# Performance work log

Hardware: AMD Instinct MI355X
Metric: run time of the kernel (lower is better)

Reference implementation:

```python
import jax, jax.numpy as jnp
import numpy as np

LN_EPS = 1e-5


def _ln(x, g, b):
    m = x.mean(-1, keepdims=True)
    v = ((x - m) ** 2).mean(-1, keepdims=True)
    return (x - m) * jax.lax.rsqrt(v + LN_EPS) * g + b


def setup_inputs() -> dict:
    key = jax.random.key(0)
    ks = jax.random.split(key, 8)
    B, S, T, Ds, Dt, H = 2, 1024, 1024, 128, 64, 64

    def w(k, shp):
        return jax.random.normal(k, shp, dtype=jnp.float32) * 0.05

    return {
        "source_features": jax.random.normal(ks[0], (B, S, Ds), dtype=jnp.float32),
        "target_features": jax.random.normal(ks[1], (B, T, Dt), dtype=jnp.float32),
        # source_adapter: Linear(Ds,H) -> LN(H) -> ReLU -> Linear(H,H)
        "sW1": w(ks[2], (Ds, H)), "sb1": jnp.zeros(H), "sg": jnp.ones(H), "sbeta": jnp.zeros(H),
        "sW2": w(ks[3], (H, H)), "sb2": jnp.zeros(H),
        # target_adapter: Linear(Dt,H) -> LN(H) -> ReLU -> Linear(H,H)
        "tW1": w(ks[4], (Dt, H)), "tb1": jnp.zeros(H), "tg": jnp.ones(H), "tbeta": jnp.zeros(H),
        "tW2": w(ks[5], (H, H)), "tb2": jnp.zeros(H),
        # city_features: Linear(2H,H) -> LN(H) -> ReLU
        "cW": w(ks[6], (2 * H, H)), "cb": jnp.zeros(H), "cg": jnp.ones(H), "cbeta": jnp.zeros(H),
        # similarity_module: Linear(H,1) -> Sigmoid
        "simW": w(ks[7], (H, 1)), "simb": jnp.zeros(1),
    }


def reference(source_features, target_features,
              sW1, sb1, sg, sbeta, sW2, sb2,
              tW1, tb1, tg, tbeta, tW2, tb2,
              cW, cb, cg, cbeta, simW, simb):
    H = sW2.shape[1]
    s_ad = jax.nn.relu(_ln(source_features @ sW1 + sb1, sg, sbeta)) @ sW2 + sb2  # [B,S,H]
    t_ad = jax.nn.relu(_ln(target_features @ tW1 + tb1, tg, tbeta)) @ tW2 + tb2  # [B,T,H]

    # concat order in torch is [target, source] on the last dim; split the
    # Linear(2H,H) weight so the [B,T,S,2H] concat is never materialized.
    cW_t, cW_s = cW[:H], cW[H:]
    pre = (t_ad @ cW_t)[:, :, None, :] + (s_ad @ cW_s)[:, None, :, :] + cb  # [B,T,S,H]
    h = jax.nn.relu(_ln(pre, cg, cbeta))
    scores = jax.nn.sigmoid((h @ simW)[..., 0] + simb[0])  # [B,T,S]

    attn = jax.nn.softmax(scores, axis=-1)
    transferred = jnp.einsum('bts,bsh->bth', attn, s_ad)
    gate = jax.nn.sigmoid(t_ad.mean(-1, keepdims=True))
    adapted = t_ad * (1.0 - gate) + transferred * gate  # hidden_dim == target_dim: no proj
    return adapted, scores
```

## Files before the change

kernel.cpp:

```cpp
#include <hip/hip_runtime.h>
#include <math.h>

#define BN 2
#define SN 1024
#define TN 1024
#define DS 128
#define DT 64
#define HN 64
#define LN_EPS 1e-5f

__device__ __forceinline__ float wave_sum(float v) {
#pragma unroll
  for (int m = 32; m >= 1; m >>= 1) v += __shfl_xor(v, m, 64);
  return v;
}

__global__ __launch_bounds__(256) void k_adapters(
    const float* __restrict__ src, const float* __restrict__ tgt,
    const float* __restrict__ sW1, const float* __restrict__ sb1,
    const float* __restrict__ sg, const float* __restrict__ sbeta,
    const float* __restrict__ sW2, const float* __restrict__ sb2,
    const float* __restrict__ tW1, const float* __restrict__ tb1,
    const float* __restrict__ tg, const float* __restrict__ tbeta,
    const float* __restrict__ tW2, const float* __restrict__ tb2,
    const float* __restrict__ cW, const float* __restrict__ cb,
    float* __restrict__ s_ad, float* __restrict__ sc, float* __restrict__ sstats,
    float* __restrict__ t_ad, float* __restrict__ tc, float* __restrict__ tstats)
{
  __shared__ float xbuf[4][DS];
  __shared__ float rbuf[4][HN];
  int w = threadIdx.x >> 6, lane = threadIdx.x & 63;

  if (blockIdx.x < 512) {
    int row = blockIdx.x * 4 + w;
    xbuf[w][lane]      = src[row * DS + lane];
    xbuf[w][lane + 64] = src[row * DS + 64 + lane];
    float a0 = 0.f, a1 = 0.f, a2_ = 0.f, a3 = 0.f;
#pragma unroll 8
    for (int k = 0; k < DS; k += 4) {
      a0  = fmaf(xbuf[w][k + 0], sW1[(k + 0) * HN + lane], a0);
      a1  = fmaf(xbuf[w][k + 1], sW1[(k + 1) * HN + lane], a1);
      a2_ = fmaf(xbuf[w][k + 2], sW1[(k + 2) * HN + lane], a2_);
      a3  = fmaf(xbuf[w][k + 3], sW1[(k + 3) * HN + lane], a3);
    }
    float h1 = ((a0 + a1) + (a2_ + a3)) + sb1[lane];
    float s1 = wave_sum(h1), s2 = wave_sum(h1 * h1);
    float m = s1 * (1.f / HN);
    float var = s2 * (1.f / HN) - m * m;
    float r = fmaxf(0.f, (h1 - m) * rsqrtf(var + LN_EPS) * sg[lane] + sbeta[lane]);
    rbuf[w][lane] = r;
    float b0 = 0.f, b1 = 0.f, b2 = 0.f, b3 = 0.f;
#pragma unroll 4
    for (int j = 0; j < HN; j += 4) {
      b0 = fmaf(rbuf[w][j + 0], sW2[(j + 0) * HN + lane], b0);
      b1 = fmaf(rbuf[w][j + 1], sW2[(j + 1) * HN + lane], b1);
      b2 = fmaf(rbuf[w][j + 2], sW2[(j + 2) * HN + lane], b2);
      b3 = fmaf(rbuf[w][j + 3], sW2[(j + 3) * HN + lane], b3);
    }
    float a2 = ((b0 + b1) + (b2 + b3)) + sb2[lane];
    s_ad[row * HN + lane] = a2;
    rbuf[w][lane] = a2;
    float c0 = 0.f, c1 = 0.f, c2 = 0.f, c3 = 0.f;
#pragma unroll 4
    for (int j = 0; j < HN; j += 4) {
      c0 = fmaf(rbuf[w][j + 0], cW[(HN + j + 0) * HN + lane], c0);
      c1 = fmaf(rbuf[w][j + 1], cW[(HN + j + 1) * HN + lane], c1);
      c2 = fmaf(rbuf[w][j + 2], cW[(HN + j + 2) * HN + lane], c2);
      c3 = fmaf(rbuf[w][j + 3], cW[(HN + j + 3) * HN + lane], c3);
    }
    float scv = (c0 + c1) + (c2 + c3);
    sc[row * HN + lane] = scv;
    float bs = wave_sum(scv), qs = wave_sum(scv * scv);
    if (lane == 0) { sstats[row * 2] = bs; sstats[row * 2 + 1] = qs; }
  } else {
    int row = (blockIdx.x - 512) * 4 + w;
    xbuf[w][lane] = tgt[row * DT + lane];
    float a0 = 0.f, a1 = 0.f, a2_ = 0.f, a3 = 0.f;
#pragma unroll 4
    for (int k = 0; k < DT; k += 4) {
      a0  = fmaf(xbuf[w][k + 0], tW1[(k + 0) * HN + lane], a0);
      a1  = fmaf(xbuf[w][k + 1], tW1[(k + 1) * HN + lane], a1);
      a2_ = fmaf(xbuf[w][k + 2], tW1[(k + 2) * HN + lane], a2_);
      a3  = fmaf(xbuf[w][k + 3], tW1[(k + 3) * HN + lane], a3);
    }
    float h1 = ((a0 + a1) + (a2_ + a3)) + tb1[lane];
    float s1 = wave_sum(h1), s2 = wave_sum(h1 * h1);
    float m = s1 * (1.f / HN);
    float var = s2 * (1.f / HN) - m * m;
    float r = fmaxf(0.f, (h1 - m) * rsqrtf(var + LN_EPS) * tg[lane] + tbeta[lane]);
    rbuf[w][lane] = r;
    float b0 = 0.f, b1 = 0.f, b2 = 0.f, b3 = 0.f;
#pragma unroll 4
    for (int j = 0; j < HN; j += 4) {
      b0 = fmaf(rbuf[w][j + 0], tW2[(j + 0) * HN + lane], b0);
      b1 = fmaf(rbuf[w][j + 1], tW2[(j + 1) * HN + lane], b1);
      b2 = fmaf(rbuf[w][j + 2], tW2[(j + 2) * HN + lane], b2);
      b3 = fmaf(rbuf[w][j + 3], tW2[(j + 3) * HN + lane], b3);
    }
    float a2 = ((b0 + b1) + (b2 + b3)) + tb2[lane];
    t_ad[row * HN + lane] = a2;
    float asum = wave_sum(a2);
    float gate = 1.f / (1.f + __expf(-asum * (1.f / HN)));
    rbuf[w][lane] = a2;
    float c0 = 0.f, c1 = 0.f, c2 = 0.f, c3 = 0.f;
#pragma unroll 4
    for (int j = 0; j < HN; j += 4) {
      c0 = fmaf(rbuf[w][j + 0], cW[(j + 0) * HN + lane], c0);
      c1 = fmaf(rbuf[w][j + 1], cW[(j + 1) * HN + lane], c1);
      c2 = fmaf(rbuf[w][j + 2], cW[(j + 2) * HN + lane], c2);
      c3 = fmaf(rbuf[w][j + 3], cW[(j + 3) * HN + lane], c3);
    }
    float tcv = ((c0 + c1) + (c2 + c3)) + cb[lane];
    tc[row * HN + lane] = tcv;
    float A = wave_sum(tcv), Q = wave_sum(tcv * tcv);
    if (lane == 0) { tstats[row * 3] = A; tstats[row * 3 + 1] = Q; tstats[row * 3 + 2] = gate; }
  }
}

__global__ __launch_bounds__(512, 4) void k_scores(
    const float* __restrict__ cg, const float* __restrict__ cbeta,
    const float* __restrict__ simW, const float* __restrict__ simb,
    const float* __restrict__ sc, const float* __restrict__ sstats,
    const float* __restrict__ tc, const float* __restrict__ tstats,
    float* __restrict__ out_scores)
{
  __shared__ float tile[128 * 64];
  int tid = threadIdx.x;
  int w = tid >> 6, lane = tid & 63;
  int sblk = blockIdx.x & 3;
  int tblk = (blockIdx.x >> 2) & 127;
  int b    = blockIdx.x >> 9;
  int t = tblk * 8 + w;
  int rt = __builtin_amdgcn_readfirstlane(b * TN + t);

  float A  = tstats[rt * 3 + 0];
  float Qt = tstats[rt * 3 + 1];
  const float* tcr = tc + rt * HN;
  float simb0 = simb[0];

  const float4* scg = (const float4*)(sc + b * SN * HN);

#pragma unroll 1
  for (int c = 0; c < 2; ++c) {
    int s0 = sblk * 256 + c * 128;
    __syncthreads();
#pragma unroll
    for (int it = 0; it < 4; ++it) {
      int j = it * 512 + tid;
      int srow = j >> 4, g = j & 15;
      float4 v = scg[(s0 + srow) * 16 + g];
      int gp = g ^ (srow & 15);
      *(float4*)&tile[srow * 64 + gp * 4] = v;
    }
    __syncthreads();

#pragma unroll 1
    for (int half = 0; half < 2; ++half) {
      int srow = half * 64 + lane;
      int s = s0 + srow;
      float2 bq = *(const float2*)&sstats[(b * SN + s) * 2];

      float D0 = 0.f, D1 = 0.f, D2 = 0.f, D3 = 0.f;
#pragma unroll
      for (int g = 0; g < 16; ++g) {
        int gp = g ^ (srow & 15);
        float4 v = *(const float4*)&tile[srow * 64 + gp * 4];
        D0 = fmaf(tcr[g * 4 + 0], v.x, D0);
        D1 = fmaf(tcr[g * 4 + 1], v.y, D1);
        D2 = fmaf(tcr[g * 4 + 2], v.z, D2);
        D3 = fmaf(tcr[g * 4 + 3], v.w, D3);
      }
      float D = (D0 + D1) + (D2 + D3);
      float mean  = (A + bq.x) * (1.f / HN);
      float e2    = (Qt + bq.y + 2.f * D) * (1.f / HN);
      float var   = e2 - mean * mean;
      float alpha = rsqrtf(var + LN_EPS);

      float dot0 = 0.f, dot1 = 0.f;
#pragma unroll
      for (int g = 0; g < 16; ++g) {
        int gp = g ^ (srow & 15);
        float4 v = *(const float4*)&tile[srow * 64 + gp * 4];
        int h = g * 4;
        {
          float P = alpha * cg[h + 0];
          float q = fmaf(-mean, P, cbeta[h + 0]);
          float n = fmaf(v.x + tcr[h + 0], P, q);
          dot0 = fmaf(fmaxf(n, 0.f), simW[h + 0], dot0);
        }
        {
          float P = alpha * cg[h + 1];
          float q = fmaf(-mean, P, cbeta[h + 1]);
          float n = fmaf(v.y + tcr[h + 1], P, q);
          dot1 = fmaf(fmaxf(n, 0.f), simW[h + 1], dot1);
        }
        {
          float P = alpha * cg[h + 2];
          float q = fmaf(-mean, P, cbeta[h + 2]);
          float n = fmaf(v.z + tcr[h + 2], P, q);
          dot0 = fmaf(fmaxf(n, 0.f), simW[h + 2], dot0);
        }
        {
          float P = alpha * cg[h + 3];
          float q = fmaf(-mean, P, cbeta[h + 3]);
          float n = fmaf(v.w + tcr[h + 3], P, q);
          dot1 = fmaf(fmaxf(n, 0.f), simW[h + 3], dot1);
        }
      }
      float dot = dot0 + dot1;
      float score = 1.f / (1.f + __expf(-(dot + simb0)));
      out_scores[rt * SN + s] = score;
    }
  }
}

__global__ __launch_bounds__(256, 4) void k_xfer(
    const float* __restrict__ scores, const float* __restrict__ s_ad,
    float* __restrict__ xpart, float* __restrict__ epart)
{
  __shared__ float eLDS[4][16][64];
  __shared__ float part[4][16][64];
  __shared__ float esum[4][16];
  int tid = threadIdx.x;
  int w = __builtin_amdgcn_readfirstlane(tid >> 6);
  int lane = tid & 63;
  int sblk = blockIdx.x & 3;
  int tblk = (blockIdx.x >> 2) & 63;
  int b    = blockIdx.x >> 8;
  int t0 = tblk * 16;
  int soff = sblk * 256 + w * 64;

#pragma unroll 4
  for (int t = 0; t < 16; ++t) {
    int rt = __builtin_amdgcn_readfirstlane(b * TN + t0 + t);
    float ev = __expf(scores[rt * SN + soff + lane]);
    eLDS[w][t][lane] = ev;
    float es = wave_sum(ev);
    if (lane == 0) esum[w][t] = es;
  }

  const float* sadb = s_ad + b * SN * HN;
  float acc[16];
#pragma unroll
  for (int t = 0; t < 16; ++t) acc[t] = 0.f;
#pragma unroll 4
  for (int si4 = 0; si4 < 16; ++si4) {
    int sbase = soff + si4 * 4;
    float sv0 = sadb[(sbase + 0) * HN + lane];
    float sv1 = sadb[(sbase + 1) * HN + lane];
    float sv2 = sadb[(sbase + 2) * HN + lane];
    float sv3 = sadb[(sbase + 3) * HN + lane];
#pragma unroll
    for (int t = 0; t < 16; ++t) {
      float4 e4 = *(const float4*)&eLDS[w][t][si4 * 4];
      acc[t] = fmaf(e4.x, sv0, acc[t]);
      acc[t] = fmaf(e4.y, sv1, acc[t]);
      acc[t] = fmaf(e4.z, sv2, acc[t]);
      acc[t] = fmaf(e4.w, sv3, acc[t]);
    }
  }

#pragma unroll
  for (int t = 0; t < 16; ++t) part[w][t][lane] = acc[t];
  __syncthreads();
#pragma unroll
  for (int k = 0; k < 4; ++k) {
    int c2 = tid + k * 256;
    int t = c2 >> 6, h = c2 & 63;
    float sum = part[0][t][h] + part[1][t][h] + part[2][t][h] + part[3][t][h];
    int rt = b * TN + t0 + t;
    xpart[(rt * 4 + sblk) * HN + h] = sum;
  }
  if (tid < 16) {
    float es = esum[0][tid] + esum[1][tid] + esum[2][tid] + esum[3][tid];
    int rt = b * TN + t0 + tid;
    epart[rt * 4 + sblk] = es;
  }
}

__global__ __launch_bounds__(256) void k_final(
    const float* __restrict__ xpart, const float* __restrict__ epart,
    const float* __restrict__ t_ad, const float* __restrict__ tstats,
    float* __restrict__ out_adapted)
{
  int tid = threadIdx.x;
  int tl = tid >> 6, h = tid & 63;
  int rt = blockIdx.x * 4 + tl;
  float x = xpart[(rt * 4 + 0) * HN + h] + xpart[(rt * 4 + 1) * HN + h]
          + xpart[(rt * 4 + 2) * HN + h] + xpart[(rt * 4 + 3) * HN + h];
  float es = epart[rt * 4 + 0] + epart[rt * 4 + 1]
           + epart[rt * 4 + 2] + epart[rt * 4 + 3];
  float tr = x / es;
  float gate = tstats[rt * 3 + 2];
  float tad = t_ad[rt * HN + h];
  out_adapted[rt * HN + h] = tad * (1.f - gate) + tr * gate;
}

extern "C" void kernel_launch(void* const* d_in, const int* in_sizes, int n_in,
                              void* d_out, int out_size, void* d_ws, size_t ws_size,
                              hipStream_t stream) {
  const float* src   = (const float*)d_in[0];
  const float* tgt   = (const float*)d_in[1];
  const float* sW1   = (const float*)d_in[2];
  const float* sb1   = (const float*)d_in[3];
  const float* sg    = (const float*)d_in[4];
  const float* sbeta = (const float*)d_in[5];
  const float* sW2   = (const float*)d_in[6];
  const float* sb2   = (const float*)d_in[7];
  const float* tW1   = (const float*)d_in[8];
  const float* tb1   = (const float*)d_in[9];
  const float* tg    = (const float*)d_in[10];
  const float* tbeta = (const float*)d_in[11];
  const float* tW2   = (const float*)d_in[12];
  const float* tb2   = (const float*)d_in[13];
  const float* cW    = (const float*)d_in[14];
  const float* cb    = (const float*)d_in[15];
  const float* cg    = (const float*)d_in[16];
  const float* cbeta = (const float*)d_in[17];
  const float* simW  = (const float*)d_in[18];
  const float* simb  = (const float*)d_in[19];

  float* ws     = (float*)d_ws;
  float* s_ad   = ws;
  float* sc     = ws + 131072;
  float* sstats = ws + 262144;
  float* t_ad   = ws + 266240;
  float* tc     = ws + 397312;
  float* tstats = ws + 528384;
  float* xpart  = ws + 534528;
  float* epart  = ws + 1058816;

  float* out_adapted = (float*)d_out;
  float* out_scores  = (float*)d_out + 131072;

  hipLaunchKernelGGL(k_adapters, dim3(1024), dim3(256), 0, stream,
                     src, tgt, sW1, sb1, sg, sbeta, sW2, sb2,
                     tW1, tb1, tg, tbeta, tW2, tb2, cW, cb,
                     s_ad, sc, sstats, t_ad, tc, tstats);
  hipLaunchKernelGGL(k_scores, dim3(BN * 128 * 4), dim3(512), 0, stream,
                     cg, cbeta, simW, simb, sc, sstats, tc, tstats, out_scores);
  hipLaunchKernelGGL(k_xfer, dim3(BN * 64 * 4), dim3(256), 0, stream,
                     out_scores, s_ad, xpart, epart);
  hipLaunchKernelGGL(k_final, dim3(512), dim3(256), 0, stream,
                     xpart, epart, t_ad, tstats, out_adapted);
}
```

Before: 182.9 us.

## Double-buffer source tile in score kernel and use packed FP32 math

Rewrites the score kernel's main loop so the source-feature tile is loaded in 64-row chunks into a double-buffered LDS array. The next chunk's global loads are issued into registers before the current chunk is computed, and a single barrier per iteration replaces the two used before. The per-element LayerNorm/ReLU/dot math is also rewritten with 2-wide vector types so the compiler can emit packed FP32 FMA/add/max instructions, and the parameter loads become float4. This aims to hide global-load latency and roughly halve VALU instruction count, at the cost of extra registers for the prefetch values.

```diff
diff --git a/kernel.cpp b/kernel.cpp
--- a/kernel.cpp
+++ b/kernel.cpp
@@ -8,6 +8,8 @@
 #define DT 64
 #define HN 64
 #define LN_EPS 1e-5f
+
+typedef float v2f __attribute__((ext_vector_type(2)));
 
 __device__ __forceinline__ float wave_sum(float v) {
 #pragma unroll
@@ -124,7 +126,7 @@
     const float* __restrict__ tc, const float* __restrict__ tstats,
     float* __restrict__ out_scores)
 {
-  __shared__ float tile[128 * 64];
+  __shared__ float tile[2][64 * 64];
   int tid = threadIdx.x;
   int w = tid >> 6, lane = tid & 63;
   int sblk = blockIdx.x & 3;
@@ -135,82 +137,101 @@
 
   float A  = tstats[rt * 3 + 0];
   float Qt = tstats[rt * 3 + 1];
-  const float* tcr = tc + rt * HN;
+  const float4* tcq = (const float4*)(tc + rt * HN);
+  const float4* cgq = (const float4*)cg;
+  const float4* cbq = (const float4*)cbeta;
+  const float4* swq = (const float4*)simW;
   float simb0 = simb[0];
 
   const float4* scg = (const float4*)(sc + b * SN * HN);
+  int s0 = sblk * 256;
+
+  int j0 = tid, j1 = 512 + tid;
+  int r0 = j0 >> 4, g0 = j0 & 15;
+  int r1 = j1 >> 4, g1 = j1 & 15;
+  int d0 = r0 * 64 + ((g0 ^ (r0 & 15)) * 4);
+  int d1 = r1 * 64 + ((g1 ^ (r1 & 15)) * 4);
+
+  {
+    float4 v0 = scg[(s0 + r0) * 16 + g0];
+    float4 v1 = scg[(s0 + r1) * 16 + g1];
+    *(float4*)&tile[0][d0] = v0;
+    *(float4*)&tile[0][d1] = v1;
+  }
+  __syncthreads();
 
 #pragma unroll 1
-  for (int c = 0; c < 2; ++c) {
-    int s0 = sblk * 256 + c * 128;
+  for (int c = 0; c < 4; ++c) {
+    float4 p0, p1;
+    if (c < 3) {
+      int sn = s0 + (c + 1) * 64;
+      p0 = scg[(sn + r0) * 16 + g0];
+      p1 = scg[(sn + r1) * 16 + g1];
+    }
+
+    const float* tb_ = &tile[c & 1][0];
+    int srow = lane;
+    int s = s0 + c * 64 + lane;
+    float2 bq = *(const float2*)&sstats[(b * SN + s) * 2];
+
+    v2f D2 = {0.f, 0.f};
+#pragma unroll
+    for (int g = 0; g < 16; ++g) {
+      float4 v = *(const float4*)&tb_[srow * 64 + ((g ^ (srow & 15)) * 4)];
+      float4 t4 = tcq[g];
+      v2f vlo = {v.x, v.y}, vhi = {v.z, v.w};
+      v2f tlo = {t4.x, t4.y}, thi = {t4.z, t4.w};
+      D2 = __builtin_elementwise_fma(tlo, vlo, D2);
+      D2 = __builtin_elementwise_fma(thi, vhi, D2);
+    }
+    float D = D2.x + D2.y;
+    float mean  = (A + bq.x) * (1.f / HN);
+    float e2    = (Qt + bq.y + 2.f * D) * (1.f / HN);
+    float var   = e2 - mean * mean;
+    float alpha = rsqrtf(var + LN_EPS);
+
+    v2f m2 = {mean, mean};
+    v2f a2 = {alpha, alpha};
+    v2f zero2 = {0.f, 0.f};
+    v2f dot2 = {0.f, 0.f};
+
+#pragma unroll
+    for (int g = 0; g < 16; ++g) {
+      float4 v  = *(const float4*)&tb_[srow * 64 + ((g ^ (srow & 15)) * 4)];
+      float4 t4 = tcq[g];
+      float4 c4 = cgq[g];
+      float4 b4 = cbq[g];
+      float4 w4 = swq[g];
+      {
+        v2f vv = {v.x, v.y}, tt = {t4.x, t4.y};
+        v2f cc = {c4.x, c4.y}, bb = {b4.x, b4.y}, ss = {w4.x, w4.y};
+        v2f u = vv + tt;
+        v2f z = u - m2;
+        v2f P = a2 * cc;
+        v2f n = __builtin_elementwise_fma(z, P, bb);
+        v2f r = __builtin_elementwise_max(n, zero2);
+        dot2 = __builtin_elementwise_fma(r, ss, dot2);
+      }
+      {
+        v2f vv = {v.z, v.w}, tt = {t4.z, t4.w};
+        v2f cc = {c4.z, c4.w}, bb = {b4.z, b4.w}, ss = {w4.z, w4.w};
+        v2f u = vv + tt;
+        v2f z = u - m2;
+        v2f P = a2 * cc;
+        v2f n = __builtin_elementwise_fma(z, P, bb);
+        v2f r = __builtin_elementwise_max(n, zero2);
+        dot2 = __builtin_elementwise_fma(r, ss, dot2);
+      }
+    }
+    float dot = dot2.x + dot2.y;
+    float score = 1.f / (1.f + __expf(-(dot + simb0)));
+    out_scores[rt * SN + s] = score;
+
+    if (c < 3) {
+      *(float4*)&tile[(c + 1) & 1][d0] = p0;
+      *(float4*)&tile[(c + 1) & 1][d1] = p1;
+    }
     __syncthreads();
-#pragma unroll
-    for (int it = 0; it < 4; ++it) {
-      int j = it * 512 + tid;
-      int srow = j >> 4, g = j & 15;
-      float4 v = scg[(s0 + srow) * 16 + g];
-      int gp = g ^ (srow & 15);
-      *(float4*)&tile[srow * 64 + gp * 4] = v;
-    }
-    __syncthreads();
-
-#pragma unroll 1
-    for (int half = 0; half < 2; ++half) {
-      int srow = half * 64 + lane;
-      int s = s0 + srow;
-      float2 bq = *(const float2*)&sstats[(b * SN + s) * 2];
-
-      float D0 = 0.f, D1 = 0.f, D2 = 0.f, D3 = 0.f;
-#pragma unroll
-      for (int g = 0; g < 16; ++g) {
-        int gp = g ^ (srow & 15);
-        float4 v = *(const float4*)&tile[srow * 64 + gp * 4];
-        D0 = fmaf(tcr[g * 4 + 0], v.x, D0);
-        D1 = fmaf(tcr[g * 4 + 1], v.y, D1);
-        D2 = fmaf(tcr[g * 4 + 2], v.z, D2);
-        D3 = fmaf(tcr[g * 4 + 3], v.w, D3);
-      }
-      float D = (D0 + D1) + (D2 + D3);
-      float mean  = (A + bq.x) * (1.f / HN);
-      float e2    = (Qt + bq.y + 2.f * D) * (1.f / HN);
-      float var   = e2 - mean * mean;
-      float alpha = rsqrtf(var + LN_EPS);
-
-      float dot0 = 0.f, dot1 = 0.f;
-#pragma unroll
-      for (int g = 0; g < 16; ++g) {
-        int gp = g ^ (srow & 15);
-        float4 v = *(const float4*)&tile[srow * 64 + gp * 4];
-        int h = g * 4;
-        {
-          float P = alpha * cg[h + 0];
-          float q = fmaf(-mean, P, cbeta[h + 0]);
-          float n = fmaf(v.x + tcr[h + 0], P, q);
-          dot0 = fmaf(fmaxf(n, 0.f), simW[h + 0], dot0);
-        }
-        {
-          float P = alpha * cg[h + 1];
-          float q = fmaf(-mean, P, cbeta[h + 1]);
-          float n = fmaf(v.y + tcr[h + 1], P, q);
-          dot1 = fmaf(fmaxf(n, 0.f), simW[h + 1], dot1);
-        }
-        {
-          float P = alpha * cg[h + 2];
-          float q = fmaf(-mean, P, cbeta[h + 2]);
-          float n = fmaf(v.z + tcr[h + 2], P, q);
-          dot0 = fmaf(fmaxf(n, 0.f), simW[h + 2], dot0);
-        }
-        {
-          float P = alpha * cg[h + 3];
-          float q = fmaf(-mean, P, cbeta[h + 3]);
-          float n = fmaf(v.w + tcr[h + 3], P, q);
-          dot1 = fmaf(fmaxf(n, 0.f), simW[h + 3], dot1);
-        }
-      }
-      float dot = dot0 + dot1;
-      float score = 1.f / (1.f + __expf(-(dot + simb0)));
-      out_scores[rt * SN + s] = score;
-    }
   }
 }
 
```

Result: faster. 169.3 us (-7.4%).
